# Kernel optimization log

Measured on AMD Instinct MI355X. Metric: run time of the kernel, lower is better.

Reference implementation:

```python
import jax, jax.numpy as jnp
import numpy as np

N_NODES = 100000  # same count for users and items
N_EDGES = 4000000
D = 64
EPS = 1e-12


def setup_inputs() -> dict:
    key = jax.random.key(0)
    ks = jax.random.split(key, 8)
    return {
        "user_feat": jax.random.normal(ks[0], (N_NODES, D), dtype=jnp.float32),
        "item_feat": jax.random.normal(ks[1], (N_NODES, D), dtype=jnp.float32),
        "norm_ui": jax.random.uniform(ks[2], (N_EDGES, 1), dtype=jnp.float32),
        "norm_iu": jax.random.uniform(ks[3], (N_EDGES, 1), dtype=jnp.float32),
        "src_ui": jax.random.randint(ks[4], (N_EDGES,), 0, N_NODES, dtype=jnp.int32),
        "dst_ui": jax.random.randint(ks[5], (N_EDGES,), 0, N_NODES, dtype=jnp.int32),
        "src_iu": jax.random.randint(ks[6], (N_EDGES,), 0, N_NODES, dtype=jnp.int32),
        "dst_iu": jax.random.randint(ks[7], (N_EDGES,), 0, N_NODES, dtype=jnp.int32),
    }


def _l2_normalize(x):
    # F.normalize(x, dim=1, p=2): x / max(||x||_2, eps)
    n = jnp.sqrt(jnp.sum(x * x, axis=1, keepdims=True))
    return x / jnp.maximum(n, EPS)


def reference(user_feat, item_feat, norm_ui, norm_iu, src_ui, dst_ui, src_iu, dst_iu):
    # per-edge gather + scale (messages), then scatter-sum to destination nodes
    item_h = jax.ops.segment_sum(norm_ui * user_feat[src_ui], dst_ui, num_segments=N_NODES)
    user_h = jax.ops.segment_sum(norm_iu * item_feat[src_iu], dst_iu, num_segments=N_NODES)
    # per-node-type L2 normalize; stack [user_h, item_h] -> [2, N, D]
    return jnp.stack([_l2_normalize(user_h), _l2_normalize(item_h)])
```

## Files before the change

### kernel.cpp

```cpp
#include <hip/hip_runtime.h>

#define DFEAT 64
#define EPS 1e-12f
#define BPB_C 256
#define MAXC 800
#define QPT 4
#define CAPA 11264


__device__ __forceinline__ unsigned pack_src_w(int s, float w) {
    unsigned u = __float_as_uint(w) + 0x8000u;
    return (((u >> 16) & 0x7FFFu) << 17) | (unsigned)s;
}
__device__ __forceinline__ int unpack_src(unsigned p) { return (int)(p & 0x1FFFFu); }
__device__ __forceinline__ float unpack_w(unsigned p) {
    return __uint_as_float(((p >> 17) & 0x7FFFu) << 16);
}

__global__ void zero_int_kernel(int* __restrict__ p, int n) {
    int i = blockIdx.x * blockDim.x + threadIdx.x;
    if (i < n) p[i] = 0;
}

__global__ __launch_bounds__(256, 6) void stageA_kernel(
        const int* __restrict__ src_ui,
        const int* __restrict__ dst_ui,
        const float* __restrict__ norm_ui,
        const int* __restrict__ src_iu,
        const int* __restrict__ dst_iu,
        const float* __restrict__ norm_iu,
        int* __restrict__ cursorC,
        unsigned* __restrict__ srcwA,
        unsigned char* __restrict__ binA,
        int n_edges, int n_nodes, int nbC, int capA) {
    __shared__ int cnt[MAXC];
    __shared__ int basearr[MAXC];
    __shared__ unsigned binstash[256 * QPT * 4];
    const int tid = threadIdx.x;
    const long long total = 2LL * n_edges;
    const long long qbase = (long long)blockIdx.x * (256 * QPT);

    for (int c = tid; c < nbC; c += 256) cnt[c] = 0;
    __syncthreads();

    for (int k = 0; k < QPT; ++k) {
        const int lq = k * 256 + tid;
        long long q = qbase + lq;
        long long g0 = q << 2;
        const int sidx = lq * 4;
        if (g0 >= total) continue;
        if (g0 + 3 < total && (g0 + 3 < n_edges || g0 >= n_edges)) {
            const bool iu = (g0 >= n_edges);
            long long e0 = iu ? (g0 - n_edges) : g0;
            int4 d = *reinterpret_cast<const int4*>((iu ? dst_iu : dst_ui) + e0);
            int boff = iu ? n_nodes : 0;
            int b0 = d.x + boff, b1 = d.y + boff, b2 = d.z + boff, b3 = d.w + boff;
            binstash[sidx + 0] = (unsigned)b0;
            binstash[sidx + 1] = (unsigned)b1;
            binstash[sidx + 2] = (unsigned)b2;
            binstash[sidx + 3] = (unsigned)b3;
            atomicAdd(&cnt[b0 >> 8], 1);
            atomicAdd(&cnt[b1 >> 8], 1);
            atomicAdd(&cnt[b2 >> 8], 1);
            atomicAdd(&cnt[b3 >> 8], 1);
        } else {
            for (long long g = g0; g < g0 + 4 && g < total; ++g) {
                int bin = (g < n_edges) ? dst_ui[g]
                                        : n_nodes + dst_iu[g - n_edges];
                binstash[sidx + (int)(g - g0)] = (unsigned)bin;
                atomicAdd(&cnt[bin >> 8], 1);
            }
        }
    }
    __syncthreads();

    for (int c = tid; c < nbC; c += 256) {
        int n = cnt[c];
        basearr[c] = (n > 0) ? atomicAdd(&cursorC[c], n) : 0;
    }
    __syncthreads();
    for (int c = tid; c < nbC; c += 256) cnt[c] = 0;
    __syncthreads();

    auto place = [&](int bin, int s, float w) {
        int bu = bin >> 8;
        int r = atomicAdd(&cnt[bu], 1);
        int pos = basearr[bu] + r;
        if (pos < capA) {
            long long slot = (long long)bu * capA + pos;
            srcwA[slot] = pack_src_w(s, w);
            binA[slot] = (unsigned char)(bin & 255);
        }
    };
    for (int k = 0; k < QPT; ++k) {
        const int lq = k * 256 + tid;
        long long q = qbase + lq;
        long long g0 = q << 2;
        const int sidx = lq * 4;
        if (g0 >= total) continue;
        if (g0 + 3 < total && (g0 + 3 < n_edges || g0 >= n_edges)) {
            const bool iu = (g0 >= n_edges);
            long long e0 = iu ? (g0 - n_edges) : g0;
            int4 s = *reinterpret_cast<const int4*>((iu ? src_iu : src_ui) + e0);
            float4 w = *reinterpret_cast<const float4*>((iu ? norm_iu : norm_ui) + e0);
            place((int)binstash[sidx + 0], s.x, w.x);
            place((int)binstash[sidx + 1], s.y, w.y);
            place((int)binstash[sidx + 2], s.z, w.z);
            place((int)binstash[sidx + 3], s.w, w.w);
        } else {
            for (long long g = g0; g < g0 + 4 && g < total; ++g) {
                int s; float w;
                if (g < n_edges) { s = src_ui[g]; w = norm_ui[g]; }
                else             { long long e = g - n_edges; s = src_iu[e]; w = norm_iu[e]; }
                place((int)binstash[sidx + (int)(g - g0)], s, w);
            }
        }
    }
}

__global__ __launch_bounds__(512, 2) void stageB_kernel(
        const int* __restrict__ cursorC,
        int* __restrict__ gcur,
        const unsigned* __restrict__ srcwA,
        const unsigned char* __restrict__ binA,
        unsigned* __restrict__ srcwB,
        int* __restrict__ startF,
        int* __restrict__ endF,
        int n_bins, int capA) {
    __shared__ int cnt[BPB_C];
    __shared__ int cnt2[BPB_C];
    __shared__ int rp[BPB_C];
    __shared__ int wtot[4];
    __shared__ int sbase;
    const int tid = threadIdx.x;
    const int lane = tid & 63;
    const int wid = tid >> 6;
    const int c = blockIdx.x;
    int m = cursorC[c];
    if (m > capA) m = capA;
    const long long js = (long long)c * capA;

    if (tid < BPB_C) { cnt[tid] = 0; cnt2[tid] = 0; }
    __syncthreads();

    for (int i = tid * 4; i < m; i += 2048) {
        if (i + 3 < m) {
            uchar4 b = *reinterpret_cast<const uchar4*>(binA + js + i);
            atomicAdd(&cnt[(int)b.x], 1);
            atomicAdd(&cnt[(int)b.y], 1);
            atomicAdd(&cnt[(int)b.z], 1);
            atomicAdd(&cnt[(int)b.w], 1);
        } else {
            for (int k = i; k < m; ++k) atomicAdd(&cnt[(int)binA[js + k]], 1);
        }
    }
    __syncthreads();

    if (tid == 0) sbase = atomicAdd(gcur, m);
    int v = 0, sc = 0;
    if (tid < BPB_C) {
        v = cnt[tid];
        sc = v;
        #pragma unroll
        for (int off = 1; off < 64; off <<= 1) {
            int y = __shfl_up(sc, off, 64);
            if (lane >= off) sc += y;
        }
        if (lane == 63) wtot[wid] = sc;
    }
    __syncthreads();
    if (tid < BPB_C) {
        int add = 0;
        for (int w = 0; w < wid; ++w) add += wtot[w];
        int excl = add + sc - v;
        rp[tid] = excl;
        int bg = c * BPB_C + tid;
        if (bg < n_bins) {
            startF[bg] = sbase + excl;
            endF[bg]   = sbase + excl + v;
        }
    }
    __syncthreads();

    for (int i = tid * 4; i < m; i += 2048) {
        if (i + 3 < m) {
            uint4 sv = *reinterpret_cast<const uint4*>(srcwA + js + i);
            uchar4 b = *reinterpret_cast<const uchar4*>(binA + js + i);
            int p0 = sbase + rp[(int)b.x] + atomicAdd(&cnt2[(int)b.x], 1);
            srcwB[p0] = sv.x;
            int p1 = sbase + rp[(int)b.y] + atomicAdd(&cnt2[(int)b.y], 1);
            srcwB[p1] = sv.y;
            int p2 = sbase + rp[(int)b.z] + atomicAdd(&cnt2[(int)b.z], 1);
            srcwB[p2] = sv.z;
            int p3 = sbase + rp[(int)b.w] + atomicAdd(&cnt2[(int)b.w], 1);
            srcwB[p3] = sv.w;
        } else {
            for (int k = i; k < m; ++k) {
                int b = (int)binA[js + k];
                int pos = sbase + rp[b] + atomicAdd(&cnt2[b], 1);
                srcwB[pos] = srcwA[js + k];
            }
        }
    }
}

__global__ __launch_bounds__(256, 8) void csr_gather_kernel(
    const float* __restrict__ user_feat,
    const float* __restrict__ item_feat,
    const int* __restrict__ startF,
    const int* __restrict__ endF,
    const unsigned* __restrict__ srcw,
    float* __restrict__ out, int n_nodes) {
    const int tid = threadIdx.x;
    const int lane = tid & 63;
    const int wid = tid >> 6;
    const int n_bins = 2 * n_nodes;
    const int r = blockIdx.x * 4 + wid;
    if (r >= n_bins) return;
    const float* feat = (r < n_nodes) ? user_feat : item_feat;
    const int js = startF[r];
    const int je = endF[r];
    float acc = 0.f;
    int j = js;
    for (; j + 16 <= je; j += 16) {
        unsigned sv[16];
        #pragma unroll
        for (int k = 0; k < 16; ++k) sv[k] = srcw[j + k];
        float fv[16];
        #pragma unroll
        for (int k = 0; k < 16; ++k)
            fv[k] = feat[(long long)unpack_src(sv[k]) * DFEAT + lane];
        #pragma unroll
        for (int k = 0; k < 16; ++k) acc += unpack_w(sv[k]) * fv[k];
    }
    for (; j + 8 <= je; j += 8) {
        unsigned sv[8];
        #pragma unroll
        for (int k = 0; k < 8; ++k) sv[k] = srcw[j + k];
        float fv[8];
        #pragma unroll
        for (int k = 0; k < 8; ++k)
            fv[k] = feat[(long long)unpack_src(sv[k]) * DFEAT + lane];
        #pragma unroll
        for (int k = 0; k < 8; ++k) acc += unpack_w(sv[k]) * fv[k];
    }
    for (; j < je; ++j) {
        unsigned s = srcw[j];
        acc += unpack_w(s) * feat[(long long)unpack_src(s) * DFEAT + lane];
    }
    float ss = acc * acc;
    #pragma unroll
    for (int o = 32; o > 0; o >>= 1) ss += __shfl_xor(ss, o, 64);
    float scale = 1.0f / fmaxf(sqrtf(ss), EPS);
    int out_row = (r < n_nodes) ? (r + n_nodes) : (r - n_nodes);
    out[(long long)out_row * DFEAT + lane] = acc * scale;
}


__global__ void zero_f32_kernel(float* __restrict__ p, int n4) {
    int i = blockIdx.x * blockDim.x + threadIdx.x;
    if (i < n4) reinterpret_cast<float4*>(p)[i] = make_float4(0.f, 0.f, 0.f, 0.f);
}

__global__ void scatter_edges_kernel(const float* __restrict__ user_feat,
                                     const float* __restrict__ item_feat,
                                     const float* __restrict__ norm_ui,
                                     const float* __restrict__ norm_iu,
                                     const int* __restrict__ src_ui,
                                     const int* __restrict__ dst_ui,
                                     const int* __restrict__ src_iu,
                                     const int* __restrict__ dst_iu,
                                     float* __restrict__ user_acc,
                                     float* __restrict__ item_acc,
                                     int n_edges) {
    long long idx = (long long)blockIdx.x * blockDim.x + threadIdx.x;
    int e = (int)(idx >> 6);
    int d = (int)(idx & 63);
    if (e < n_edges) {
        int s = src_ui[e];
        int t = dst_ui[e];
        atomicAdd(&item_acc[(long long)t * DFEAT + d],
                  norm_ui[e] * user_feat[(long long)s * DFEAT + d]);
    } else {
        e -= n_edges;
        if (e < n_edges) {
            int s = src_iu[e];
            int t = dst_iu[e];
            atomicAdd(&user_acc[(long long)t * DFEAT + d],
                      norm_iu[e] * item_feat[(long long)s * DFEAT + d]);
        }
    }
}

__global__ void normalize_rows_kernel(float* __restrict__ buf, int n_rows) {
    int gid = blockIdx.x * blockDim.x + threadIdx.x;
    int row = gid >> 6;
    int lane = gid & 63;
    if (row >= n_rows) return;
    long long off = (long long)row * DFEAT + lane;
    float x = buf[off];
    float ss = x * x;
    #pragma unroll
    for (int o = 32; o > 0; o >>= 1) ss += __shfl_xor(ss, o, 64);
    float scale = 1.0f / fmaxf(sqrtf(ss), EPS);
    buf[off] = x * scale;
}

extern "C" void kernel_launch(void* const* d_in, const int* in_sizes, int n_in,
                              void* d_out, int out_size, void* d_ws, size_t ws_size,
                              hipStream_t stream) {
    const float* user_feat = (const float*)d_in[0];
    const float* item_feat = (const float*)d_in[1];
    const float* norm_ui   = (const float*)d_in[2];
    const float* norm_iu   = (const float*)d_in[3];
    const int* src_ui = (const int*)d_in[4];
    const int* dst_ui = (const int*)d_in[5];
    const int* src_iu = (const int*)d_in[6];
    const int* dst_iu = (const int*)d_in[7];

    const int n_nodes = in_sizes[0] / DFEAT;
    const int n_edges = in_sizes[4];
    const int n_bins  = 2 * n_nodes;
    const int nbC     = (n_bins + BPB_C - 1) / BPB_C;
    const long long total = 2LL * n_edges;

    const long long mean_per_region = total / (nbC > 0 ? nbC : 1);
    long long capA_ll = (mean_per_region + mean_per_region / 8 + 127) & ~15LL;
    if (capA_ll < 256) capA_ll = 256;
    const int capA = (int)capA_ll;

    auto align256 = [](size_t x) { return (x + 255) & ~(size_t)255; };
    const size_t o_curC  = 0;
    const size_t o_stF   = align256(o_curC + ((size_t)nbC + 1) * 4);
    const size_t o_enF   = align256(o_stF + (size_t)n_bins * 4);
    const size_t o_srcwB = align256(o_enF + (size_t)n_bins * 4);
    const size_t ws_need = o_srcwB + (size_t)total * 4;
    const size_t out_bytes = (size_t)n_bins * DFEAT * sizeof(float);
    const size_t out_need  = (size_t)nbC * capA * 5;

    if (nbC <= MAXC && n_nodes <= (1 << 17) &&
        ws_size >= ws_need && out_bytes >= out_need) {
        int* cursorC    = (int*)((char*)d_ws + o_curC);
        int* gcur       = cursorC + nbC;
        int* startF     = (int*)((char*)d_ws + o_stF);
        int* endF       = (int*)((char*)d_ws + o_enF);
        unsigned* srcwB = (unsigned*)((char*)d_ws + o_srcwB);
        unsigned* srcwA      = (unsigned*)d_out;
        unsigned char* binA  = (unsigned char*)d_out + (size_t)nbC * capA * 4;

        const long long rpb = 256LL * QPT * 4;
        const int pblocks = (int)((total + rpb - 1) / rpb);

        zero_int_kernel<<<(nbC + 256) / 256, 256, 0, stream>>>(cursorC, nbC + 1);
        stageA_kernel<<<pblocks, 256, 0, stream>>>(
            src_ui, dst_ui, norm_ui, src_iu, dst_iu, norm_iu,
            cursorC, srcwA, binA, n_edges, n_nodes, nbC, capA);
        stageB_kernel<<<nbC, 512, 0, stream>>>(
            cursorC, gcur, srcwA, binA, srcwB, startF, endF, n_bins, capA);
        csr_gather_kernel<<<(n_bins + 3) / 4, 256, 0, stream>>>(
            user_feat, item_feat, startF, endF, srcwB, (float*)d_out, n_nodes);
    } else {
        float* user_acc = (float*)d_out;
        float* item_acc = user_acc + (size_t)n_nodes * DFEAT;
        const long long out_elems = (long long)n_bins * DFEAT;
        const int n4 = (int)(out_elems / 4);
        zero_f32_kernel<<<(n4 + 255) / 256, 256, 0, stream>>>(user_acc, n4);
        const long long total_threads = 2LL * n_edges * DFEAT;
        scatter_edges_kernel<<<(int)((total_threads + 255) / 256), 256, 0, stream>>>(
            user_feat, item_feat, norm_ui, norm_iu,
            src_ui, dst_ui, src_iu, dst_iu, user_acc, item_acc, n_edges);
        const long long norm_threads = (long long)n_bins * DFEAT;
        normalize_rows_kernel<<<(int)((norm_threads + 255) / 256), 256, 0, stream>>>(
            user_acc, n_bins);
    }
}
```

Baseline: 662.0 us.

## Reuse histogram atomic ranks in bucketing passes instead of second atomic pass

Stage A now records each edge's rank returned by the counting atomic, packed into the upper bits of the shared stash, and stage B records ranks and bin ids in new shared arrays. The second pass of each kernel then computes destinations directly without a second round of shared-memory atomics or a counter reset. The CSR gather kernel also marks the row bounds as wave-uniform via readfirstlane. The trade-off is extra shared memory in stage B (about 35 KB), and a launch-bounds change that asks for higher occupancy which that shared memory may not allow; a capA bound check is added to the guard.

```diff
diff --git a/kernel.cpp b/kernel.cpp
--- a/kernel.cpp
+++ b/kernel.cpp
@@ -5,7 +5,7 @@
 #define BPB_C 256
 #define MAXC 800
 #define QPT 4
-#define CAPA 11264
+#define CAPB 11648
 
 
 __device__ __forceinline__ unsigned pack_src_w(int s, float w) {
@@ -55,20 +55,20 @@
             int4 d = *reinterpret_cast<const int4*>((iu ? dst_iu : dst_ui) + e0);
             int boff = iu ? n_nodes : 0;
             int b0 = d.x + boff, b1 = d.y + boff, b2 = d.z + boff, b3 = d.w + boff;
-            binstash[sidx + 0] = (unsigned)b0;
-            binstash[sidx + 1] = (unsigned)b1;
-            binstash[sidx + 2] = (unsigned)b2;
-            binstash[sidx + 3] = (unsigned)b3;
-            atomicAdd(&cnt[b0 >> 8], 1);
-            atomicAdd(&cnt[b1 >> 8], 1);
-            atomicAdd(&cnt[b2 >> 8], 1);
-            atomicAdd(&cnt[b3 >> 8], 1);
+            int r0 = atomicAdd(&cnt[b0 >> 8], 1);
+            int r1 = atomicAdd(&cnt[b1 >> 8], 1);
+            int r2 = atomicAdd(&cnt[b2 >> 8], 1);
+            int r3 = atomicAdd(&cnt[b3 >> 8], 1);
+            binstash[sidx + 0] = (unsigned)b0 | ((unsigned)r0 << 18);
+            binstash[sidx + 1] = (unsigned)b1 | ((unsigned)r1 << 18);
+            binstash[sidx + 2] = (unsigned)b2 | ((unsigned)r2 << 18);
+            binstash[sidx + 3] = (unsigned)b3 | ((unsigned)r3 << 18);
         } else {
             for (long long g = g0; g < g0 + 4 && g < total; ++g) {
                 int bin = (g < n_edges) ? dst_ui[g]
                                         : n_nodes + dst_iu[g - n_edges];
-                binstash[sidx + (int)(g - g0)] = (unsigned)bin;
-                atomicAdd(&cnt[bin >> 8], 1);
+                int rk = atomicAdd(&cnt[bin >> 8], 1);
+                binstash[sidx + (int)(g - g0)] = (unsigned)bin | ((unsigned)rk << 18);
             }
         }
     }
@@ -79,13 +79,12 @@
         basearr[c] = (n > 0) ? atomicAdd(&cursorC[c], n) : 0;
     }
     __syncthreads();
-    for (int c = tid; c < nbC; c += 256) cnt[c] = 0;
-    __syncthreads();
-
-    auto place = [&](int bin, int s, float w) {
+
+    auto place = [&](unsigned st, int s, float w) {
+        int bin  = (int)(st & 0x3FFFFu);
+        int rank = (int)(st >> 18);
         int bu = bin >> 8;
-        int r = atomicAdd(&cnt[bu], 1);
-        int pos = basearr[bu] + r;
+        int pos = basearr[bu] + rank;
         if (pos < capA) {
             long long slot = (long long)bu * capA + pos;
             srcwA[slot] = pack_src_w(s, w);
@@ -103,22 +102,22 @@
             long long e0 = iu ? (g0 - n_edges) : g0;
             int4 s = *reinterpret_cast<const int4*>((iu ? src_iu : src_ui) + e0);
             float4 w = *reinterpret_cast<const float4*>((iu ? norm_iu : norm_ui) + e0);
-            place((int)binstash[sidx + 0], s.x, w.x);
-            place((int)binstash[sidx + 1], s.y, w.y);
-            place((int)binstash[sidx + 2], s.z, w.z);
-            place((int)binstash[sidx + 3], s.w, w.w);
+            place(binstash[sidx + 0], s.x, w.x);
+            place(binstash[sidx + 1], s.y, w.y);
+            place(binstash[sidx + 2], s.z, w.z);
+            place(binstash[sidx + 3], s.w, w.w);
         } else {
             for (long long g = g0; g < g0 + 4 && g < total; ++g) {
                 int s; float w;
                 if (g < n_edges) { s = src_ui[g]; w = norm_ui[g]; }
                 else             { long long e = g - n_edges; s = src_iu[e]; w = norm_iu[e]; }
-                place((int)binstash[sidx + (int)(g - g0)], s, w);
+                place(binstash[sidx + (int)(g - g0)], s, w);
             }
         }
     }
 }
 
-__global__ __launch_bounds__(512, 2) void stageB_kernel(
+__global__ __launch_bounds__(512, 8) void stageB_kernel(
         const int* __restrict__ cursorC,
         int* __restrict__ gcur,
         const unsigned* __restrict__ srcwA,
@@ -128,10 +127,11 @@
         int* __restrict__ endF,
         int n_bins, int capA) {
     __shared__ int cnt[BPB_C];
-    __shared__ int cnt2[BPB_C];
     __shared__ int rp[BPB_C];
     __shared__ int wtot[4];
     __shared__ int sbase;
+    __shared__ unsigned short rankL[CAPB];
+    __shared__ unsigned char  binL[CAPB];
     const int tid = threadIdx.x;
     const int lane = tid & 63;
     const int wid = tid >> 6;
@@ -140,18 +140,26 @@
     if (m > capA) m = capA;
     const long long js = (long long)c * capA;
 
-    if (tid < BPB_C) { cnt[tid] = 0; cnt2[tid] = 0; }
+    if (tid < BPB_C) cnt[tid] = 0;
     __syncthreads();
 
     for (int i = tid * 4; i < m; i += 2048) {
         if (i + 3 < m) {
             uchar4 b = *reinterpret_cast<const uchar4*>(binA + js + i);
-            atomicAdd(&cnt[(int)b.x], 1);
-            atomicAdd(&cnt[(int)b.y], 1);
-            atomicAdd(&cnt[(int)b.z], 1);
-            atomicAdd(&cnt[(int)b.w], 1);
+            int r0 = atomicAdd(&cnt[(int)b.x], 1);
+            int r1 = atomicAdd(&cnt[(int)b.y], 1);
+            int r2 = atomicAdd(&cnt[(int)b.z], 1);
+            int r3 = atomicAdd(&cnt[(int)b.w], 1);
+            rankL[i + 0] = (unsigned short)r0; binL[i + 0] = b.x;
+            rankL[i + 1] = (unsigned short)r1; binL[i + 1] = b.y;
+            rankL[i + 2] = (unsigned short)r2; binL[i + 2] = b.z;
+            rankL[i + 3] = (unsigned short)r3; binL[i + 3] = b.w;
         } else {
-            for (int k = i; k < m; ++k) atomicAdd(&cnt[(int)binA[js + k]], 1);
+            for (int k = i; k < m; ++k) {
+                unsigned char bb = binA[js + k];
+                int rk = atomicAdd(&cnt[(int)bb], 1);
+                rankL[k] = (unsigned short)rk; binL[k] = bb;
+            }
         }
     }
     __syncthreads();
@@ -185,19 +193,17 @@
     for (int i = tid * 4; i < m; i += 2048) {
         if (i + 3 < m) {
             uint4 sv = *reinterpret_cast<const uint4*>(srcwA + js + i);
-            uchar4 b = *reinterpret_cast<const uchar4*>(binA + js + i);
-            int p0 = sbase + rp[(int)b.x] + atomicAdd(&cnt2[(int)b.x], 1);
+            int p0 = sbase + rp[(int)binL[i + 0]] + (int)rankL[i + 0];
+            int p1 = sbase + rp[(int)binL[i + 1]] + (int)rankL[i + 1];
+            int p2 = sbase + rp[(int)binL[i + 2]] + (int)rankL[i + 2];
+            int p3 = sbase + rp[(int)binL[i + 3]] + (int)rankL[i + 3];
             srcwB[p0] = sv.x;
-            int p1 = sbase + rp[(int)b.y] + atomicAdd(&cnt2[(int)b.y], 1);
             srcwB[p1] = sv.y;
-            int p2 = sbase + rp[(int)b.z] + atomicAdd(&cnt2[(int)b.z], 1);
             srcwB[p2] = sv.z;
-            int p3 = sbase + rp[(int)b.w] + atomicAdd(&cnt2[(int)b.w], 1);
             srcwB[p3] = sv.w;
         } else {
             for (int k = i; k < m; ++k) {
-                int b = (int)binA[js + k];
-                int pos = sbase + rp[b] + atomicAdd(&cnt2[b], 1);
+                int pos = sbase + rp[(int)binL[k]] + (int)rankL[k];
                 srcwB[pos] = srcwA[js + k];
             }
         }
@@ -218,8 +224,8 @@
     const int r = blockIdx.x * 4 + wid;
     if (r >= n_bins) return;
     const float* feat = (r < n_nodes) ? user_feat : item_feat;
-    const int js = startF[r];
-    const int je = endF[r];
+    const int js = __builtin_amdgcn_readfirstlane(startF[r]);
+    const int je = __builtin_amdgcn_readfirstlane(endF[r]);
     float acc = 0.f;
     int j = js;
     for (; j + 16 <= je; j += 16) {
@@ -338,7 +344,7 @@
     const size_t out_bytes = (size_t)n_bins * DFEAT * sizeof(float);
     const size_t out_need  = (size_t)nbC * capA * 5;
 
-    if (nbC <= MAXC && n_nodes <= (1 << 17) &&
+    if (nbC <= MAXC && n_nodes <= (1 << 17) && capA <= CAPB &&
         ws_size >= ws_need && out_bytes >= out_need) {
         int* cursorC    = (int*)((char*)d_ws + o_curC);
         int* gcur       = cursorC + nbC;
```

After: 651.1 us. Within noise of the previous version (-1.6%).
